# Kernel optimization log

Measured on AMD Instinct MI355X. Metric: run time of the kernel, lower is better.

## Reference

```python
import jax, jax.numpy as jnp
import numpy as np
import math

D = 768
H = 12
HD = D // H  # 64


def setup_inputs() -> dict:
    key = jax.random.key(0)
    ks = jax.random.split(key, 8)
    B, S = 32, 127
    desc = jax.random.normal(ks[0], (B, S, D), dtype=jnp.float32)
    nv = jax.random.normal(ks[1], (B, S + 1, D), dtype=jnp.float32)
    def xavier(k, shape):
        fan_in, fan_out = shape[1], shape[0]
        gain = 1.0 / math.sqrt(2.0)
        limit = gain * math.sqrt(6.0 / (fan_in + fan_out))
        return jax.random.uniform(k, shape, jnp.float32, -limit, limit)
    Wq = xavier(ks[2], (D, D)); bq = jnp.zeros((D,), jnp.float32)
    Wk = xavier(ks[3], (D, D)); bk = jnp.zeros((D,), jnp.float32)
    Wv = xavier(ks[4], (D, D)); bv = jnp.zeros((D,), jnp.float32)
    # attn_proj: Linear(3*head_dim, 1)
    Wa = xavier(ks[5], (1, 3 * HD))[0]  # [3*HD]
    ba = jnp.zeros((), jnp.float32)
    return {
        "desc_embeddings": desc,
        "name_value_embeddings": nv,
        "Wq": Wq, "bq": bq, "Wk": Wk, "bk": bk, "Wv": Wv, "bv": bv,
        "Wa": Wa, "ba": ba,
    }


def _forward(desc_embeddings, name_value_embeddings, Wq, bq, Wk, bk, Wv, bv, Wa, ba):
    B, new_seq, _ = name_value_embeddings.shape
    S = new_seq - 1

    # adjacency: var-var all ones, CLS->Var row = 1, Var->CLS col = 0, CLS->CLS = 0
    adj = jnp.zeros((new_seq, new_seq), jnp.float32)
    adj = adj.at[1:, 1:].set(1.0)
    adj = adj.at[0, 1:].set(1.0)
    adj = jnp.broadcast_to(adj, (B, new_seq, new_seq))

    # q,k,v: [B, H, new_seq, HD]
    def proj(W, b):
        y = name_value_embeddings @ W.T + b
        return y.reshape(B, new_seq, H, HD).transpose(0, 2, 1, 3)
    q = proj(Wq, bq); k = proj(Wk, bk); v = proj(Wv, bv)

    # attn_proj weight split: [q_part | k_part | edge_part], each [HD]
    wq_a, wk_a, we_a = Wa[:HD], Wa[HD:2 * HD], Wa[2 * HD:]

    # q/k scalar contributions per (b,h,i) and (b,h,j)
    lq = jnp.einsum('bhid,d->bhi', q, wq_a)  # [B,H,new_seq]
    lk = jnp.einsum('bhjd,d->bhj', k, wk_a)  # [B,H,new_seq]

    # edge_attr[b,i,j] per head h (head slice of concat[node_i_desc, node_j_desc]):
    # edge vector = concat(desc_i, desc_j)[h*HD:(h+1)*HD] viewed as [H, HD] of 2D dims.
    # concat(desc_i, desc_j) has 2D dims -> reshaped to [H, HD] means head h takes
    # slice [h*HD:(h+1)*HD] of the 2D-dim concat. Heads 0..H/2-1 come from desc_i,
    # heads H/2..H-1 come from desc_j. Compute edge dot with we_a accordingly.
    # desc_full[b,t] : [B,S,D]. Build per-head contributions:
    # for h < H//2: edge slice = desc_i[h*HD:(h+1)*HD]  -> depends only on i
    # for h >= H//2: edge slice = desc_j[(h-H//2)*HD:(h-H//2+1)*HD] -> depends only on j
    desc_heads = desc_embeddings.reshape(B, S, H // 2, 2 * HD)  # wrong split; do directly
    # Direct: per head h, slice indices into the 2D concat vector
    dh = desc_embeddings.reshape(B, S, H, HD)  # desc split into H chunks of HD (covers D = H*HD)
    # concat(desc_i,desc_j) reshaped to [H,HD]: heads 0..H/2-1 use dh_i[:, :, h],
    # heads H/2..H-1 use dh_j[:, :, h - H/2]
    e_dot = jnp.einsum('bshd,d->bsh', dh, jnp.broadcast_to(we_a, (HD,)))  # placeholder, recompute per head below
    # per-head edge scalar contribution for var-var edges:
    ei = jnp.einsum('bshd,d->bhs', dh, we_a)  # contribution if head slice comes from desc at position s
    Hh = H // 2
    # var-var logits edge part: for h<Hh depends on i; for h>=Hh depends on j
    le_i = ei[:, :Hh, :]   # [B,Hh,S] depends on i (row)
    le_j = ei[:, Hh:, :]   # [B,Hh,S] depends on j (col)

    # CLS edges: cls_edge_attr = concat(desc, desc) at position t (the var index)
    # row 0 (CLS->var j): edge = concat(desc_j, desc_j) -> head h slice:
    #   h<Hh: dh_j[h]; h>=Hh: dh_j[h-Hh]  -> scalar ei[b,h,j] with h mapped
    e_cls = jnp.concatenate([ei[:, :Hh, :], ei[:, :Hh, :]], axis=1) * 0  # init
    e_cls = jnp.concatenate([le_i, le_i], axis=1)  # [B,H,S]: head h<Hh uses dh[h], h>=Hh uses dh[h-Hh]
    # note ei[:, :Hh] corresponds to dh chunks 0..Hh-1 ; for h>=Hh slice is dh[h-Hh] -> same le_i

    # Assemble full logits [B,H,new_seq,new_seq]
    logits = lq[:, :, :, None] + lk[:, :, None, :]
    # edge contributions (only where adj==1; edge_attr zeroed elsewhere by mask mult)
    edge = jnp.zeros((B, H, new_seq, new_seq), jnp.float32)
    # var-var block [1:,1:]
    ev = jnp.zeros((B, H, S, S), jnp.float32)
    ev = ev + jnp.pad(le_i, ((0, 0), (0, Hh), (0, 0)))[:, :, :, None] * 0  # keep shapes
    ev_i = jnp.concatenate([le_i, jnp.zeros_like(le_j)], axis=1)  # h<Hh: i-dependent
    ev_j = jnp.concatenate([jnp.zeros_like(le_i), le_j], axis=1)  # h>=Hh: j-dependent
    ev = ev_i[:, :, :, None] + ev_j[:, :, None, :]  # [B,H,S,S]
    edge = edge.at[:, :, 1:, 1:].set(ev)
    # CLS row (0, 1:): cls_edge = concat(desc_j,desc_j); j = column var
    edge = edge.at[:, :, 0, 1:].set(e_cls)
    # CLS col (1:, 0): cls_edge = concat(desc_i,desc_i) BUT adj[:,1:,0]=0 so edge_attr
    # multiplied by adj -> zero; also masked out. edge stays 0, but torch zeroes it too.
    # mask edge by adjacency (edge_attr *= adj)
    edge = edge * adj[:, None, :, :]
    logits = logits + edge + ba

    mask = (adj[:, None, :, :] == 0).astype(jnp.float32) * -1e9
    logits = logits + mask
    attn = jax.nn.softmax(logits, axis=-1)  # [B,H,new_seq,new_seq]
    ctx = jnp.einsum('bhij,bhjd->bhid', attn, v)
    basis_outputs = ctx.transpose(0, 2, 1, 3)  # [B,new_seq,H,HD]
    return basis_outputs, attn


def reference(desc_embeddings, name_value_embeddings, Wq, bq, Wk, bk, Wv, bv, Wa, ba):
    return _forward(desc_embeddings, name_value_embeddings, Wq, bq, Wk, bk, Wv, bv, Wa, ba)
```

## Files before the change

### kernel.cpp

```cpp
#include <hip/hip_runtime.h>

#define NB 32
#define NS 128
#define SD 127
#define ND 768
#define NH 12
#define HD 64

__device__ inline float wredSum(float v){
  #pragma unroll
  for (int off=32; off>0; off>>=1) v += __shfl_xor(v, off);
  return v;
}
__device__ inline float wredMax(float v){
  #pragma unroll
  for (int off=32; off>0; off>>=1) v = fmaxf(v, __shfl_xor(v, off));
  return v;
}

__global__ __launch_bounds__(256)
void fold_k(const float* __restrict__ Wk, const float* __restrict__ bk,
            const float* __restrict__ Wa, float* __restrict__ uk,
            float* __restrict__ bkdot){
  int blk = blockIdx.x;
  int h = blk/12, cb = blk%12;
  int t = threadIdx.x;
  int c0 = t & 63, dg = t >> 6;
  const float* base = Wk + (size_t)(h*HD + dg*16)*ND + cb*64 + c0;
  float acc = 0.f;
  #pragma unroll
  for (int i=0;i<16;++i) acc += base[(size_t)i*ND] * Wa[64 + dg*16 + i];
  __shared__ float red[4][64];
  red[dg][c0] = acc;
  __syncthreads();
  if (dg==0) uk[h*ND + cb*64 + c0] = red[0][c0]+red[1][c0]+red[2][c0]+red[3][c0];
  if (blk==0 && t < NH){
    float a = 0.f;
    for (int d=0; d<64; ++d) a += bk[t*HD+d]*Wa[64+d];
    bkdot[t] = a;
  }
}

__global__ __launch_bounds__(256)
void lk_ei(const float* __restrict__ nv, const float* __restrict__ desc,
           const float* __restrict__ uk, const float* __restrict__ bkdot,
           const float* __restrict__ Wa,
           float* __restrict__ lk, float* __restrict__ ei){
  __shared__ float sh[ND];
  int blk = blockIdx.x;
  int wave = threadIdx.x >> 6, lane = threadIdx.x & 63;
  if (blk < NB*NS){
    int b = blk >> 7, j = blk & 127;
    const float* row = nv + (size_t)blk * ND;
    for (int c = threadIdx.x; c < ND; c += 256) sh[c] = row[c];
    __syncthreads();
    #pragma unroll
    for (int hh=0; hh<3; ++hh){
      int h = wave*3 + hh;
      float acc = 0.f;
      #pragma unroll
      for (int k=0; k<12; ++k) acc += sh[lane+64*k]*uk[h*ND + lane+64*k];
      acc = wredSum(acc);
      if (lane==0) lk[(b*NH + h)*NS + j] = acc + bkdot[h];
    }
  } else {
    int bs = blk - NB*NS;
    int b = bs / SD, s = bs % SD;
    float wea = Wa[128 + lane];
    const float* row = desc + (size_t)bs * ND;
    #pragma unroll
    for (int hh=0; hh<3; ++hh){
      int h = wave + hh*4;
      float v = row[h*HD + lane] * wea;
      v = wredSum(v);
      if (lane==0) ei[(b*NH + h)*NS + s] = v;
    }
  }
}

__global__ __launch_bounds__(256)
void msoft(const float* __restrict__ nv, const float* __restrict__ lk,
           const float* __restrict__ ei, float* __restrict__ m_part){
  int blk = blockIdx.x;
  int b = blk >> 3, jg = blk & 7;
  int t = threadIdx.x, wave = t >> 6, lane = t & 63;
  __shared__ float slk[NH][NS];
  __shared__ float sei[NH][NS];
  __shared__ float wf[24][NS];
  for (int i=t; i<NH*NS; i+=256) ((float*)slk)[i] = lk[(size_t)b*NH*NS + i];
  for (int i=t; i<NH*NS; i+=256){
    int h = i >> 7, s = i & 127;
    sei[h][s] = (s < SD) ? ei[((size_t)b*NH + h)*NS + s] : 0.f;
  }
  __syncthreads();
  #pragma unroll
  for (int rr=0; rr<6; ++rr){
    int r = wave*6 + rr;
    int h = r >> 1, which = r & 1;
    const float* eirow = (which==0) ? sei[h%6] : sei[h];
    float g = (which==0) ? 1.f : (h>=6 ? 1.f : 0.f);
    float x0 = (lane>=1) ? slk[h][lane] + g*eirow[lane-1] : -3.0e38f;
    float x1 = slk[h][lane+64] + g*eirow[lane+63];
    float mm = wredMax(fmaxf(x0,x1));
    float e0 = (lane>=1) ? __expf(x0-mm) : 0.f;
    float e1 = __expf(x1-mm);
    float s  = wredSum(e0+e1);
    float inv = 1.f/s;
    wf[r][lane]    = e0*inv;
    wf[r][lane+64] = e1*inv;
  }
  __syncthreads();
  if (t < 192){
    const float4* nvb = (const float4*)(nv + ((size_t)b*NS + jg*16)*ND);
    float4 acc[24];
    #pragma unroll
    for (int r=0; r<24; ++r) acc[r] = make_float4(0.f,0.f,0.f,0.f);
    #pragma unroll 2
    for (int jj=0; jj<16; ++jj){
      float4 x = nvb[jj*192 + t];
      int j = jg*16 + jj;
      #pragma unroll
      for (int r=0; r<24; ++r){
        float wr = wf[r][j];
        acc[r].x += wr*x.x; acc[r].y += wr*x.y;
        acc[r].z += wr*x.z; acc[r].w += wr*x.w;
      }
    }
    #pragma unroll
    for (int r=0; r<24; ++r)
      ((float4*)(m_part + ((size_t)(b*24 + r)*8 + jg)*ND))[t] = acc[r];
  }
}

__global__ __launch_bounds__(512)
void proj_write(const float* __restrict__ m_part, const float* __restrict__ Wv,
                const float* __restrict__ bv, const float* __restrict__ lk,
                const float* __restrict__ ei, float* __restrict__ out){
  int bh = blockIdx.x;
  int b = bh / NH, h = bh % NH;
  int t = threadIdx.x, wave = t >> 6, lane = t & 63;
  __shared__ float msum[2][ND];
  __shared__ float w0[NS], w1[NS];
  __shared__ float cvec[2][HD];

  if (wave < 2){
    const float* lkrow = lk + (size_t)bh*NS;
    const float* eirow = ei + ((size_t)b*NH + (wave==0 ? (h%6) : h))*NS;
    float g = (wave==0) ? 1.f : (h>=6 ? 1.f : 0.f);
    float x0 = (lane>=1) ? lkrow[lane] + g*eirow[lane-1] : -3.0e38f;
    float x1 = lkrow[lane+64] + g*eirow[lane+63];
    float mm = wredMax(fmaxf(x0,x1));
    float e0 = (lane>=1) ? __expf(x0-mm) : 0.f;
    float e1 = __expf(x1-mm);
    float s  = wredSum(e0+e1);
    float inv = 1.f/s;
    float* wd = wave ? w1 : w0;
    wd[lane]    = e0*inv;
    wd[lane+64] = e1*inv;
  }
  for (int i=t; i<2*ND; i+=512){
    int rl = (i >= ND);
    int c  = i - rl*ND;
    const float* mp = m_part + ((size_t)(b*24 + h*2 + rl)*8)*ND + c;
    float s = 0.f;
    #pragma unroll
    for (int g8=0; g8<8; ++g8) s += mp[(size_t)g8*ND];
    msum[rl][c] = s;
  }
  __syncthreads();
  #pragma unroll
  for (int dd=0; dd<8; ++dd){
    int d = wave*8 + dd;
    const float* wvr = Wv + (size_t)(h*HD + d)*ND;
    float p0=0.f, p1=0.f;
    #pragma unroll
    for (int k=0; k<12; ++k){
      float wv = wvr[lane + 64*k];
      p0 += wv*msum[0][lane + 64*k];
      p1 += wv*msum[1][lane + 64*k];
    }
    p0 = wredSum(p0); p1 = wredSum(p1);
    if (lane==0){
      float bb = bv[h*HD + d];
      cvec[0][d] = p0 + bb;
      cvec[1][d] = p1 + bb;
    }
  }
  __syncthreads();
  float4* ao = (float4*)(out + (size_t)NB*NS*ND + (size_t)bh*NS*NS);
  for (int idx=t; idx<4096; idx+=512){
    int i = idx>>5, q = idx&31;
    const float* src = (i==0) ? w0 : w1;
    float4 v = { src[q*4], src[q*4+1], src[q*4+2], src[q*4+3] };
    ao[idx] = v;
  }
  float* bo = out + (size_t)b*NS*ND + h*HD;
  for (int idx=t; idx<2048; idx+=512){
    int i = idx>>4, q = idx&15;
    const float* src = (i==0) ? cvec[0] : cvec[1];
    float4 v = { src[q*4], src[q*4+1], src[q*4+2], src[q*4+3] };
    *(float4*)(bo + (size_t)i*ND + q*4) = v;
  }
}

extern "C" void kernel_launch(void* const* d_in, const int* in_sizes, int n_in,
                              void* d_out, int out_size, void* d_ws, size_t ws_size,
                              hipStream_t stream) {
  const float* desc = (const float*)d_in[0];
  const float* nv   = (const float*)d_in[1];
  const float* Wk   = (const float*)d_in[4];
  const float* bk   = (const float*)d_in[5];
  const float* Wv   = (const float*)d_in[6];
  const float* bv   = (const float*)d_in[7];
  const float* Wa   = (const float*)d_in[8];
  float* out = (float*)d_out;
  float* ws  = (float*)d_ws;

  float* uk     = ws;
  float* bkdot  = ws + 9216;
  float* ei     = ws + 9232;
  float* lkbuf  = ws + 58384;
  float* m_part = ws + 107536;

  fold_k    <<<144,  256, 0, stream>>>(Wk, bk, Wa, uk, bkdot);
  lk_ei     <<<8160, 256, 0, stream>>>(nv, desc, uk, bkdot, Wa, lkbuf, ei);
  msoft     <<<256,  256, 0, stream>>>(nv, lkbuf, ei, m_part);
  proj_write<<<384,  512, 0, stream>>>(m_part, Wv, bv, lkbuf, ei, out);
}
```

Measured before the change: 139.8 us.

## Fuse four kernels into one persistent kernel with grid-wide atomic barriers

Replaces the four separate launches with a single 256-block persistent kernel that separates its phases with software grid barriers built on atomic counters reset by a memset. The lk phase now processes four rows per iteration, keeping the folded Wk vectors in registers. Attention-matrix writes move into the softmax phase. This removes launch gaps and inter-kernel drains, but spin barriers cost time and deadlock if all 256 blocks cannot be co-resident; the later phases also run with fewer threads per block.

```diff
diff --git a/kernel.cpp b/kernel.cpp
--- a/kernel.cpp
+++ b/kernel.cpp
@@ -6,6 +6,7 @@
 #define ND 768
 #define NH 12
 #define HD 64
+#define GRID 256
 
 __device__ inline float wredSum(float v){
   #pragma unroll
@@ -18,188 +19,206 @@
   return v;
 }
 
+__device__ inline void gridbar(int* cnt){
+  __syncthreads();
+  if (threadIdx.x == 0){
+    __threadfence();
+    atomicAdd(cnt, 1);
+    while (atomicAdd(cnt, 0) < GRID) __builtin_amdgcn_s_sleep(2);
+    __threadfence();
+  }
+  __syncthreads();
+}
+
 __global__ __launch_bounds__(256)
-void fold_k(const float* __restrict__ Wk, const float* __restrict__ bk,
-            const float* __restrict__ Wa, float* __restrict__ uk,
-            float* __restrict__ bkdot){
-  int blk = blockIdx.x;
-  int h = blk/12, cb = blk%12;
-  int t = threadIdx.x;
-  int c0 = t & 63, dg = t >> 6;
-  const float* base = Wk + (size_t)(h*HD + dg*16)*ND + cb*64 + c0;
-  float acc = 0.f;
-  #pragma unroll
-  for (int i=0;i<16;++i) acc += base[(size_t)i*ND] * Wa[64 + dg*16 + i];
-  __shared__ float red[4][64];
-  red[dg][c0] = acc;
-  __syncthreads();
-  if (dg==0) uk[h*ND + cb*64 + c0] = red[0][c0]+red[1][c0]+red[2][c0]+red[3][c0];
-  if (blk==0 && t < NH){
+void mega(const float* __restrict__ desc, const float* __restrict__ nv,
+          const float* __restrict__ Wk, const float* __restrict__ bk,
+          const float* __restrict__ Wv, const float* __restrict__ bv,
+          const float* __restrict__ Wa,
+          int* __restrict__ bar, float* __restrict__ uk, float* __restrict__ bkdot,
+          float* __restrict__ lk, float* __restrict__ ei,
+          float* __restrict__ m_part, float* __restrict__ out){
+  __shared__ __align__(16) float S[6144];
+  int blk = blockIdx.x, t = threadIdx.x, wave = t>>6, lane = t&63;
+
+  if (blk < 144){
+    float (*red)[64] = (float(*)[64])S;
+    int h = blk/12, cb = blk%12;
+    int c0 = t & 63, dg = t >> 6;
+    const float* base = Wk + (size_t)(h*HD + dg*16)*ND + cb*64 + c0;
+    float acc = 0.f;
+    #pragma unroll
+    for (int i=0;i<16;++i) acc += base[(size_t)i*ND] * Wa[64 + dg*16 + i];
+    red[dg][c0] = acc;
+    __syncthreads();
+    if (dg==0) uk[h*ND + cb*64 + c0] = red[0][c0]+red[1][c0]+red[2][c0]+red[3][c0];
+  }
+  if (blk == 144 && t < NH){
     float a = 0.f;
     for (int d=0; d<64; ++d) a += bk[t*HD+d]*Wa[64+d];
     bkdot[t] = a;
   }
-}
-
-__global__ __launch_bounds__(256)
-void lk_ei(const float* __restrict__ nv, const float* __restrict__ desc,
-           const float* __restrict__ uk, const float* __restrict__ bkdot,
-           const float* __restrict__ Wa,
-           float* __restrict__ lk, float* __restrict__ ei){
-  __shared__ float sh[ND];
-  int blk = blockIdx.x;
-  int wave = threadIdx.x >> 6, lane = threadIdx.x & 63;
-  if (blk < NB*NS){
-    int b = blk >> 7, j = blk & 127;
-    const float* row = nv + (size_t)blk * ND;
-    for (int c = threadIdx.x; c < ND; c += 256) sh[c] = row[c];
-    __syncthreads();
+  {
+    float wea = Wa[128 + lane];
+    for (int task = blk; task < NB*SD; task += GRID){
+      int b = task / SD, s = task % SD;
+      const float* row = desc + (size_t)task * ND;
+      #pragma unroll
+      for (int hh=0; hh<3; ++hh){
+        int h = wave + hh*4;
+        float v = row[h*HD + lane] * wea;
+        v = wredSum(v);
+        if (lane==0) ei[(size_t)(b*NH + h)*NS + s] = v;
+      }
+    }
+  }
+  gridbar(bar + 0);
+
+  {
+    float ukr[3][12], bkd[3];
     #pragma unroll
     for (int hh=0; hh<3; ++hh){
       int h = wave*3 + hh;
-      float acc = 0.f;
-      #pragma unroll
-      for (int k=0; k<12; ++k) acc += sh[lane+64*k]*uk[h*ND + lane+64*k];
-      acc = wredSum(acc);
-      if (lane==0) lk[(b*NH + h)*NS + j] = acc + bkdot[h];
-    }
-  } else {
-    int bs = blk - NB*NS;
-    int b = bs / SD, s = bs % SD;
-    float wea = Wa[128 + lane];
-    const float* row = desc + (size_t)bs * ND;
-    #pragma unroll
-    for (int hh=0; hh<3; ++hh){
-      int h = wave + hh*4;
-      float v = row[h*HD + lane] * wea;
-      v = wredSum(v);
-      if (lane==0) ei[(b*NH + h)*NS + s] = v;
-    }
-  }
-}
-
-__global__ __launch_bounds__(256)
-void msoft(const float* __restrict__ nv, const float* __restrict__ lk,
-           const float* __restrict__ ei, float* __restrict__ m_part){
-  int blk = blockIdx.x;
-  int b = blk >> 3, jg = blk & 7;
-  int t = threadIdx.x, wave = t >> 6, lane = t & 63;
-  __shared__ float slk[NH][NS];
-  __shared__ float sei[NH][NS];
-  __shared__ float wf[24][NS];
-  for (int i=t; i<NH*NS; i+=256) ((float*)slk)[i] = lk[(size_t)b*NH*NS + i];
-  for (int i=t; i<NH*NS; i+=256){
-    int h = i >> 7, s = i & 127;
-    sei[h][s] = (s < SD) ? ei[((size_t)b*NH + h)*NS + s] : 0.f;
-  }
-  __syncthreads();
-  #pragma unroll
-  for (int rr=0; rr<6; ++rr){
-    int r = wave*6 + rr;
-    int h = r >> 1, which = r & 1;
-    const float* eirow = (which==0) ? sei[h%6] : sei[h];
-    float g = (which==0) ? 1.f : (h>=6 ? 1.f : 0.f);
-    float x0 = (lane>=1) ? slk[h][lane] + g*eirow[lane-1] : -3.0e38f;
-    float x1 = slk[h][lane+64] + g*eirow[lane+63];
-    float mm = wredMax(fmaxf(x0,x1));
-    float e0 = (lane>=1) ? __expf(x0-mm) : 0.f;
-    float e1 = __expf(x1-mm);
-    float s  = wredSum(e0+e1);
-    float inv = 1.f/s;
-    wf[r][lane]    = e0*inv;
-    wf[r][lane+64] = e1*inv;
-  }
-  __syncthreads();
-  if (t < 192){
-    const float4* nvb = (const float4*)(nv + ((size_t)b*NS + jg*16)*ND);
-    float4 acc[24];
-    #pragma unroll
-    for (int r=0; r<24; ++r) acc[r] = make_float4(0.f,0.f,0.f,0.f);
-    #pragma unroll 2
-    for (int jj=0; jj<16; ++jj){
-      float4 x = nvb[jj*192 + t];
-      int j = jg*16 + jj;
-      #pragma unroll
-      for (int r=0; r<24; ++r){
-        float wr = wf[r][j];
-        acc[r].x += wr*x.x; acc[r].y += wr*x.y;
-        acc[r].z += wr*x.z; acc[r].w += wr*x.w;
-      }
-    }
-    #pragma unroll
-    for (int r=0; r<24; ++r)
-      ((float4*)(m_part + ((size_t)(b*24 + r)*8 + jg)*ND))[t] = acc[r];
-  }
-}
-
-__global__ __launch_bounds__(512)
-void proj_write(const float* __restrict__ m_part, const float* __restrict__ Wv,
-                const float* __restrict__ bv, const float* __restrict__ lk,
-                const float* __restrict__ ei, float* __restrict__ out){
-  int bh = blockIdx.x;
-  int b = bh / NH, h = bh % NH;
-  int t = threadIdx.x, wave = t >> 6, lane = t & 63;
-  __shared__ float msum[2][ND];
-  __shared__ float w0[NS], w1[NS];
-  __shared__ float cvec[2][HD];
-
-  if (wave < 2){
-    const float* lkrow = lk + (size_t)bh*NS;
-    const float* eirow = ei + ((size_t)b*NH + (wave==0 ? (h%6) : h))*NS;
-    float g = (wave==0) ? 1.f : (h>=6 ? 1.f : 0.f);
-    float x0 = (lane>=1) ? lkrow[lane] + g*eirow[lane-1] : -3.0e38f;
-    float x1 = lkrow[lane+64] + g*eirow[lane+63];
-    float mm = wredMax(fmaxf(x0,x1));
-    float e0 = (lane>=1) ? __expf(x0-mm) : 0.f;
-    float e1 = __expf(x1-mm);
-    float s  = wredSum(e0+e1);
-    float inv = 1.f/s;
-    float* wd = wave ? w1 : w0;
-    wd[lane]    = e0*inv;
-    wd[lane+64] = e1*inv;
-  }
-  for (int i=t; i<2*ND; i+=512){
-    int rl = (i >= ND);
-    int c  = i - rl*ND;
-    const float* mp = m_part + ((size_t)(b*24 + h*2 + rl)*8)*ND + c;
-    float s = 0.f;
-    #pragma unroll
-    for (int g8=0; g8<8; ++g8) s += mp[(size_t)g8*ND];
-    msum[rl][c] = s;
-  }
-  __syncthreads();
-  #pragma unroll
-  for (int dd=0; dd<8; ++dd){
-    int d = wave*8 + dd;
-    const float* wvr = Wv + (size_t)(h*HD + d)*ND;
-    float p0=0.f, p1=0.f;
-    #pragma unroll
-    for (int k=0; k<12; ++k){
-      float wv = wvr[lane + 64*k];
-      p0 += wv*msum[0][lane + 64*k];
-      p1 += wv*msum[1][lane + 64*k];
-    }
-    p0 = wredSum(p0); p1 = wredSum(p1);
-    if (lane==0){
-      float bb = bv[h*HD + d];
-      cvec[0][d] = p0 + bb;
-      cvec[1][d] = p1 + bb;
-    }
-  }
-  __syncthreads();
-  float4* ao = (float4*)(out + (size_t)NB*NS*ND + (size_t)bh*NS*NS);
-  for (int idx=t; idx<4096; idx+=512){
-    int i = idx>>5, q = idx&31;
-    const float* src = (i==0) ? w0 : w1;
-    float4 v = { src[q*4], src[q*4+1], src[q*4+2], src[q*4+3] };
-    ao[idx] = v;
-  }
-  float* bo = out + (size_t)b*NS*ND + h*HD;
-  for (int idx=t; idx<2048; idx+=512){
-    int i = idx>>4, q = idx&15;
-    const float* src = (i==0) ? cvec[0] : cvec[1];
-    float4 v = { src[q*4], src[q*4+1], src[q*4+2], src[q*4+3] };
-    *(float4*)(bo + (size_t)i*ND + q*4) = v;
+      bkd[hh] = bkdot[h];
+      #pragma unroll
+      for (int k=0;k<12;++k) ukr[hh][k] = uk[h*ND + lane + 64*k];
+    }
+    for (int it = blk; it < 1024; it += GRID){
+      int j0 = it*4;
+      const float4* src = (const float4*)(nv + (size_t)j0*ND);
+      ((float4*)S)[t]     = src[t];
+      ((float4*)S)[t+256] = src[t+256];
+      ((float4*)S)[t+512] = src[t+512];
+      __syncthreads();
+      float acc[12];
+      #pragma unroll
+      for (int rr=0; rr<4; ++rr){
+        #pragma unroll
+        for (int hh=0; hh<3; ++hh){
+          float a = 0.f;
+          #pragma unroll
+          for (int k=0;k<12;++k) a += S[rr*ND + lane + 64*k]*ukr[hh][k];
+          acc[rr*3+hh] = a;
+        }
+      }
+      #pragma unroll
+      for (int i=0;i<12;++i) acc[i] = wredSum(acc[i]);
+      if (lane == 0){
+        int b = j0 >> 7, jb = j0 & 127;
+        #pragma unroll
+        for (int rr=0; rr<4; ++rr){
+          #pragma unroll
+          for (int hh=0; hh<3; ++hh){
+            int h = wave*3 + hh;
+            lk[(size_t)(b*NH + h)*NS + jb + rr] = acc[rr*3+hh] + bkd[hh];
+          }
+        }
+      }
+      __syncthreads();
+    }
+  }
+  gridbar(bar + 1);
+
+  {
+    int b = blk >> 3, jg = blk & 7;
+    float* slk = S;
+    float* sei = S + 1536;
+    float (*wf)[NS] = (float(*)[NS])(S + 3072);
+    for (int i=t; i<1536; i+=256) slk[i] = lk[(size_t)b*1536 + i];
+    for (int i=t; i<1536; i+=256) sei[i] = ei[(size_t)b*1536 + i];
+    __syncthreads();
+    #pragma unroll
+    for (int rr=0; rr<6; ++rr){
+      int r = wave*6 + rr;
+      int h = r >> 1, which = r & 1;
+      const float* eirow = (which==0) ? (sei + (h%6)*NS) : (sei + h*NS);
+      float g = (which==0) ? 1.f : (h>=6 ? 1.f : 0.f);
+      float x0 = (lane>=1) ? slk[h*NS+lane] + g*eirow[lane-1] : -3.0e38f;
+      float x1 = slk[h*NS+lane+64] + g*eirow[lane+63];
+      float mm = wredMax(fmaxf(x0,x1));
+      float e0 = (lane>=1) ? __expf(x0-mm) : 0.f;
+      float e1 = __expf(x1-mm);
+      float s  = wredSum(e0+e1);
+      float inv = 1.f/s;
+      wf[r][lane]    = e0*inv;
+      wf[r][lane+64] = e1*inv;
+    }
+    __syncthreads();
+    if (t < 192){
+      const float4* nvb = (const float4*)(nv + ((size_t)b*NS + jg*16)*ND);
+      float4 acc[24];
+      #pragma unroll
+      for (int r=0;r<24;++r) acc[r] = make_float4(0.f,0.f,0.f,0.f);
+      #pragma unroll 2
+      for (int jj=0; jj<16; ++jj){
+        float4 x = nvb[jj*192 + t];
+        int j = jg*16 + jj;
+        #pragma unroll
+        for (int r=0;r<24;++r){
+          float wr = wf[r][j];
+          acc[r].x += wr*x.x; acc[r].y += wr*x.y;
+          acc[r].z += wr*x.z; acc[r].w += wr*x.w;
+        }
+      }
+      #pragma unroll
+      for (int r=0;r<24;++r)
+        ((float4*)(m_part + ((size_t)(b*24 + r)*8 + jg)*ND))[t] = acc[r];
+    }
+    float* abase = out + (size_t)NB*NS*ND + (size_t)(b*NH)*NS*NS;
+    for (int idx=t; idx<6144; idx+=256){
+      int h = idx >> 9;
+      int rem = idx & 511;
+      int il = rem >> 5, q = rem & 31;
+      int i = jg*16 + il;
+      const float* srcw = (i==0) ? wf[h*2] : wf[h*2+1];
+      float4 v = { srcw[q*4], srcw[q*4+1], srcw[q*4+2], srcw[q*4+3] };
+      ((float4*)(abase + (size_t)h*NS*NS))[i*32 + q] = v;
+    }
+  }
+  gridbar(bar + 2);
+
+  for (int task = blk; task < NB*NH; task += GRID){
+    int b = task / NH, h = task % NH;
+    float* msum0 = S;
+    float* msum1 = S + ND;
+    float* cvec  = S + 2*ND;
+    for (int i=t; i<2*ND; i+=256){
+      int rl = (i >= ND);
+      int c  = i - rl*ND;
+      const float* mp = m_part + ((size_t)(b*24 + h*2 + rl)*8)*ND + c;
+      float s = 0.f;
+      #pragma unroll
+      for (int g8=0; g8<8; ++g8) s += mp[(size_t)g8*ND];
+      (rl ? msum1 : msum0)[c] = s;
+    }
+    __syncthreads();
+    #pragma unroll
+    for (int dd=0; dd<16; ++dd){
+      int d = wave*16 + dd;
+      const float* wvr = Wv + (size_t)(h*HD + d)*ND;
+      float p0=0.f, p1=0.f;
+      #pragma unroll
+      for (int k=0; k<12; ++k){
+        float wv = wvr[lane + 64*k];
+        p0 += wv*msum0[lane + 64*k];
+        p1 += wv*msum1[lane + 64*k];
+      }
+      p0 = wredSum(p0); p1 = wredSum(p1);
+      if (lane==0){
+        float bb = bv[h*HD + d];
+        cvec[d]    = p0 + bb;
+        cvec[64+d] = p1 + bb;
+      }
+    }
+    __syncthreads();
+    float* bo = out + (size_t)b*NS*ND + h*HD;
+    for (int idx=t; idx<2048; idx+=256){
+      int i = idx>>4, q = idx&15;
+      const float* srcc = (i==0) ? cvec : cvec+64;
+      float4 v = { srcc[q*4], srcc[q*4+1], srcc[q*4+2], srcc[q*4+3] };
+      *(float4*)(bo + (size_t)i*ND + q*4) = v;
+    }
+    __syncthreads();
   }
 }
 
@@ -213,17 +232,17 @@
   const float* Wv   = (const float*)d_in[6];
   const float* bv   = (const float*)d_in[7];
   const float* Wa   = (const float*)d_in[8];
-  float* out = (float*)d_out;
-  float* ws  = (float*)d_ws;
-
-  float* uk     = ws;
-  float* bkdot  = ws + 9216;
-  float* ei     = ws + 9232;
-  float* lkbuf  = ws + 58384;
-  float* m_part = ws + 107536;
-
-  fold_k    <<<144,  256, 0, stream>>>(Wk, bk, Wa, uk, bkdot);
-  lk_ei     <<<8160, 256, 0, stream>>>(nv, desc, uk, bkdot, Wa, lkbuf, ei);
-  msoft     <<<256,  256, 0, stream>>>(nv, lkbuf, ei, m_part);
-  proj_write<<<384,  512, 0, stream>>>(m_part, Wv, bv, lkbuf, ei, out);
-}
+  float* out  = (float*)d_out;
+  float* base = (float*)d_ws;
+
+  int*   bar    = (int*)d_ws;
+  float* uk     = base + 16;
+  float* bkdot  = base + 9232;
+  float* lkbuf  = base + 9248;
+  float* eibuf  = base + 58400;
+  float* m_part = base + 107552;
+
+  hipMemsetAsync(d_ws, 0, 64, stream);
+  mega<<<GRID, 256, 0, stream>>>(desc, nv, Wk, bk, Wv, bv, Wa,
+                                 bar, uk, bkdot, lkbuf, eibuf, m_part, out);
+}
```

Result: slower. 236.6 us (+69.2%).
